# Kernel optimization log

Measured on AMD Instinct MI355X. Metric: run time of the kernel, lower is better.

Reference implementation:

```python
import jax, jax.numpy as jnp
import numpy as np

TEMPERATURE = 0.1
NORM_EPS = 1e-12          # F.normalize default eps
SMALL_VAL = float(np.finfo(np.float32).tiny)  # pytorch-metric-learning small_val(float32)
NEG_INF = float(np.finfo(np.float32).min)     # c_f.neg_inf for masked logsumexp


def setup_inputs() -> dict:
    key = jax.random.key(0)
    k1, k2 = jax.random.split(key)
    N, D = 8192, 128
    emb = jax.random.normal(k1, (N, D), dtype=jnp.float32)
    labels = jax.random.randint(k2, (N,), 0, 1000, dtype=jnp.int64)
    return {"emb": emb, "labels": labels}


def reference(emb, labels):
    N = emb.shape[0]
    # F.normalize(emb, dim=1): x / max(||x||, eps)
    norms = jnp.linalg.norm(emb, axis=1, keepdims=True)
    x = emb / jnp.maximum(norms, NORM_EPS)

    # cosine similarity matrix [N, N], scaled by temperature
    mat = jnp.matmul(x, x.T) / TEMPERATURE

    same = labels[:, None] == labels[None, :]
    diag = jnp.eye(N, dtype=bool)
    pos_mask = same & ~diag          # same label, i != j
    keep_mask = ~diag                # pos + neg (all off-diagonal)

    # numerical stability: subtract detached row max (over full row, incl. diagonal)
    mat_max = jax.lax.stop_gradient(jnp.max(mat, axis=1, keepdims=True))
    mat = mat - mat_max

    # masked logsumexp over off-diagonal entries
    masked = jnp.where(keep_mask, mat, NEG_INF)
    denom = jax.nn.logsumexp(masked, axis=1, keepdims=True)  # [N, 1]

    log_prob = mat - denom
    pos_f = pos_mask.astype(mat.dtype)
    mean_log_prob_pos = jnp.sum(pos_f * log_prob, axis=1) / (
        jnp.sum(pos_f, axis=1) + SMALL_VAL
    )
    losses = -mean_log_prob_pos  # per-element losses
    # SumReducer: sum over elements
    return jnp.sum(losses)
```

## Files before the change

kernel.cpp:

```cpp
#include <hip/hip_runtime.h>
#include <hip/hip_bf16.h>


typedef __bf16 bf16_t;
typedef __bf16 bf16x2 __attribute__((ext_vector_type(2)));
typedef __bf16 bf16x8 __attribute__((ext_vector_type(8)));
typedef float f32x16 __attribute__((ext_vector_type(16)));

#define NN 8192
#define DIM 128
#define NB 256
#define SEGS 32
#define SMALL_VAL 1.17549435e-38f
#define L2E10 14.4269504089f
#define LN2 0.69314718056f

__device__ inline size_t swz(int row, int lane) {
    int f = lane >> 3, hh = (lane >> 2) & 1, j = (lane & 3) << 1;
    return ((size_t)(row >> 5) * 4096) + f * 512 + hh * 256 + (row & 31) * 8 + j;
}

__global__ __launch_bounds__(256) void norm_csum(const float* __restrict__ emb,
                                                 const int* __restrict__ labels,
                                                 bf16_t* __restrict__ xsw,
                                                 float* __restrict__ cd_arr,
                                                 float* __restrict__ sd_arr,
                                                 float* __restrict__ cm1_arr,
                                                 float* __restrict__ se_acc,
                                                 float* __restrict__ out) {
    __shared__ float cs[DIM];
    __shared__ int rowlist[96];
    __shared__ int nrows;
    int cls = blockIdx.x;
    int wv = threadIdx.x >> 6, lane = threadIdx.x & 63;
    if (threadIdx.x < DIM) cs[threadIdx.x] = 0.f;
    if (threadIdx.x == 0) nrows = 0;
    if (threadIdx.x < 8) se_acc[cls * 8 + threadIdx.x] = 0.f;
    if (cls == 0 && threadIdx.x == 0) *out = 0.f;
    __syncthreads();

    float s0 = 0.f, s1 = 0.f;
    const int4* lab4 = (const int4*)(labels + wv * 2048);
#pragma unroll
    for (int it = 0; it < 8; ++it) {
        int4 l = lab4[it * 64 + lane];
        int base = wv * 2048 + it * 256;
#pragma unroll
        for (int cmp = 0; cmp < 4; ++cmp) {
            int li = (cmp == 0) ? l.x : (cmp == 1) ? l.y : (cmp == 2) ? l.z : l.w;
            unsigned long long m = __ballot(li == cls);
            while (m) {
                int bb = __builtin_ctzll(m);
                m &= m - 1;
                int row = base + 4 * bb + cmp;
                float2 v = ((const float2*)emb)[row * 64 + lane];
                float ss = fmaf(v.x, v.x, v.y * v.y);
#pragma unroll
                for (int mm = 1; mm < 64; mm <<= 1) ss += __shfl_xor(ss, mm, 64);
                float inv = 1.0f / fmaxf(sqrtf(ss), 1e-12f);
                bf16x2 o; o.x = (bf16_t)(v.x * inv); o.y = (bf16_t)(v.y * inv);
                *(bf16x2*)(xsw + swz(row, lane)) = o;
                s0 += (float)o.x; s1 += (float)o.y;
                if (lane == 0) {
                    int idx = atomicAdd(&nrows, 1);
                    if (idx < 96) rowlist[idx] = row;
                }
            }
        }
    }
    atomicAdd(&cs[2 * lane], s0);
    atomicAdd(&cs[2 * lane + 1], s1);
    __syncthreads();
    int n = nrows;
    for (int k = wv; k < n; k += 4) {
        int row = rowlist[k];
        bf16x2 xv = *(const bf16x2*)(xsw + swz(row, lane));
        float x0 = (float)xv.x, x1 = (float)xv.y;
        float cdp = fmaf(x0, cs[2 * lane], x1 * cs[2 * lane + 1]);
        float sdp = fmaf(x0, x0, x1 * x1);
#pragma unroll
        for (int mm = 1; mm < 64; mm <<= 1) {
            cdp += __shfl_xor(cdp, mm, 64);
            sdp += __shfl_xor(sdp, mm, 64);
        }
        if (lane == 0) {
            cd_arr[row] = cdp; sd_arr[row] = sdp; cm1_arr[row] = (float)(n - 1);
        }
    }
}

__global__ __launch_bounds__(256, 4) void main_kernel(const bf16_t* __restrict__ xsw,
                                                      float* __restrict__ se_acc) {
    int wid  = blockIdx.x * 4 + (threadIdx.x >> 6);
    int lane = threadIdx.x & 63;
    int I = wid >> 5, s = wid & 31;
    int NT = NB - I;
    int t0 = (NT * s) >> 5, t1 = (NT * (s + 1)) >> 5;
    if (t0 == t1) return;

    int c = lane & 31, h = lane >> 5;
    int laneoff = h * 256 + c * 8;

    const bf16_t* abase = xsw + (size_t)I * 4096 + laneoff;
    bf16x8 a[8];
#pragma unroll
    for (int f = 0; f < 8; ++f) a[f] = *(const bf16x8*)(abase + f * 512);

    float se[16];
#pragma unroll
    for (int r = 0; r < 16; ++r) se[r] = 0.f;

    for (int t = t0; t < t1; ++t) {
        int J = I + t;
        const bf16_t* bbase = xsw + (size_t)J * 4096 + laneoff;
        bf16x8 b[8];
#pragma unroll
        for (int f = 0; f < 8; ++f) b[f] = *(const bf16x8*)(bbase + f * 512);
        f32x16 acc;
#pragma unroll
        for (int r = 0; r < 16; ++r) acc[r] = 0.f;
#pragma unroll
        for (int f = 0; f < 8; ++f)
            acc = __builtin_amdgcn_mfma_f32_32x32x16_bf16(a[f], b[f], acc, 0, 0, 0);

        if (J == I) {
#pragma unroll
            for (int r = 0; r < 16; ++r) {
                bool isdiag = c == ((r & 3) + 8 * (r >> 2) + 4 * h);
                float e = isdiag ? 0.f
                                 : __builtin_amdgcn_exp2f(fmaf(acc[r], L2E10, -L2E10));
                se[r] += e;
            }
        } else {
            float c0 = 0.f, c1 = 0.f, c2 = 0.f, c3 = 0.f;
#pragma unroll
            for (int r = 0; r < 16; ++r) {
                float e = __builtin_amdgcn_exp2f(fmaf(acc[r], L2E10, -L2E10));
                se[r] += e;
                if ((r & 3) == 0) c0 += e; else if ((r & 3) == 1) c1 += e;
                else if ((r & 3) == 2) c2 += e; else c3 += e;
            }
            float v = (c0 + c1) + (c2 + c3);
            v += __shfl_xor(v, 32, 64);
            if (h == 0) atomicAdd(&se_acc[J * 32 + c], v);
        }
    }

#pragma unroll
    for (int r = 0; r < 16; ++r) {
        float vv = se[r];
#pragma unroll
        for (int m = 1; m < 32; m <<= 1) vv += __shfl_xor(vv, m, 64);
        se[r] = vv;
    }
    if (c == 0) {
        int rowbase = I * 32 + 4 * h;
#pragma unroll
        for (int r = 0; r < 16; ++r)
            atomicAdd(&se_acc[rowbase + (r & 3) + 8 * (r >> 2)], se[r]);
    }
}

__global__ __launch_bounds__(256) void finalize_kernel(const float* __restrict__ se_acc,
                                                       const float* __restrict__ cd_arr,
                                                       const float* __restrict__ sd_arr,
                                                       const float* __restrict__ cm1_arr,
                                                       float* __restrict__ out) {
    __shared__ float part[4];
    int i = blockIdx.x * 256 + threadIdx.x;
    float sd = sd_arr[i], cd = cd_arr[i], cm1 = cm1_arr[i];
    float sev  = fmaxf(se_acc[i], 1e-30f);
    float lse  = fmaf(__builtin_amdgcn_logf(sev), LN2, 10.f);
    float loss = (cm1 * lse - 10.f * (cd - sd)) / (cm1 + SMALL_VAL);
#pragma unroll
    for (int m = 1; m < 64; m <<= 1) loss += __shfl_xor(loss, m, 64);
    int wv = threadIdx.x >> 6;
    if ((threadIdx.x & 63) == 0) part[wv] = loss;
    __syncthreads();
    if (threadIdx.x == 0) atomicAdd(out, part[0] + part[1] + part[2] + part[3]);
}

extern "C" void kernel_launch(void* const* d_in, const int* in_sizes, int n_in,
                              void* d_out, int out_size, void* d_ws, size_t ws_size,
                              hipStream_t stream) {
    const float* emb  = (const float*)d_in[0];
    const int* labels = (const int*)d_in[1];

    char* ws = (char*)d_ws;
    bf16_t* xsw = (bf16_t*)ws;
    float* se   = (float*)(ws + (size_t)NN * DIM * 2);
    float* cd   = se + NN;
    float* sd   = cd + NN;
    float* cm1  = sd + NN;

    norm_csum<<<1024, 256, 0, stream>>>(emb, labels, xsw, cd, sd, cm1, se, (float*)d_out);
    main_kernel<<<NB * SEGS / 4, 256, 0, stream>>>(xsw, se);
    finalize_kernel<<<NN / 256, 256, 0, stream>>>(se, cd, sd, cm1, (float*)d_out);
}
```

Baseline: 103.2 us.

## Fuse finalize into main kernel via last-block reduction and double-buffer B loads

The separate finalize kernel is removed. Each main_kernel block increments a done counter, and the last block to finish computes the per-row loss and writes the sum, which saves one kernel launch. The loop over B tiles now uses two register buffers so the next tile's global loads are in flight while the current MFMA and exp work runs. Launch bounds drop from 4 to 3 blocks per CU to make room for the extra registers, at the cost of occupancy, and the final reduction now runs serially on a single block.

```diff
diff --git a/kernel.cpp b/kernel.cpp
--- a/kernel.cpp
+++ b/kernel.cpp
@@ -11,6 +11,7 @@
 #define DIM 128
 #define NB 256
 #define SEGS 32
+#define NBLK (NB * SEGS / 4)
 #define SMALL_VAL 1.17549435e-38f
 #define L2E10 14.4269504089f
 #define LN2 0.69314718056f
@@ -27,7 +28,7 @@
                                                  float* __restrict__ sd_arr,
                                                  float* __restrict__ cm1_arr,
                                                  float* __restrict__ se_acc,
-                                                 float* __restrict__ out) {
+                                                 int* __restrict__ done) {
     __shared__ float cs[DIM];
     __shared__ int rowlist[96];
     __shared__ int nrows;
@@ -36,7 +37,7 @@
     if (threadIdx.x < DIM) cs[threadIdx.x] = 0.f;
     if (threadIdx.x == 0) nrows = 0;
     if (threadIdx.x < 8) se_acc[cls * 8 + threadIdx.x] = 0.f;
-    if (cls == 0 && threadIdx.x == 0) *out = 0.f;
+    if (cls == 0 && threadIdx.x == 0) *done = 0;
     __syncthreads();
 
     float s0 = 0.f, s1 = 0.f;
@@ -89,95 +90,114 @@
     }
 }
 
-__global__ __launch_bounds__(256, 4) void main_kernel(const bf16_t* __restrict__ xsw,
-                                                      float* __restrict__ se_acc) {
+#define LDB(dst, J_) do {                                                        \
+    const bf16_t* p_ = xsw + (size_t)(J_) * 4096 + laneoff;                      \
+    _Pragma("unroll")                                                            \
+    for (int f_ = 0; f_ < 8; ++f_) dst[f_] = *(const bf16x8*)(p_ + f_ * 512);    \
+} while (0)
+
+#define TILE(bb, J_) do {                                                        \
+    f32x16 acc_;                                                                 \
+    _Pragma("unroll")                                                            \
+    for (int r_ = 0; r_ < 16; ++r_) acc_[r_] = 0.f;                              \
+    _Pragma("unroll")                                                            \
+    for (int f_ = 0; f_ < 8; ++f_)                                               \
+        acc_ = __builtin_amdgcn_mfma_f32_32x32x16_bf16(a[f_], bb[f_], acc_, 0, 0, 0); \
+    if ((J_) == I) {                        \
+        _Pragma("unroll")                                                        \
+        for (int r_ = 0; r_ < 16; ++r_) {                                        \
+            bool isd_ = c == ((r_ & 3) + 8 * (r_ >> 2) + 4 * h);                 \
+            se[r_] += isd_ ? 0.f                                                 \
+                           : __builtin_amdgcn_exp2f(fmaf(acc_[r_], L2E10, -L2E10)); \
+        }                                                                        \
+    } else {                                \
+        float c0_=0.f, c1_=0.f, c2_=0.f, c3_=0.f;                                \
+        _Pragma("unroll")                                                        \
+        for (int r_ = 0; r_ < 16; ++r_) {                                        \
+            float e_ = __builtin_amdgcn_exp2f(fmaf(acc_[r_], L2E10, -L2E10));    \
+            se[r_] += e_;                                                        \
+            if ((r_&3)==0) c0_+=e_; else if ((r_&3)==1) c1_+=e_;                 \
+            else if ((r_&3)==2) c2_+=e_; else c3_+=e_;                           \
+        }                                                                        \
+        float v_ = (c0_ + c1_) + (c2_ + c3_);                                    \
+        v_ += __shfl_xor(v_, 32, 64);                                            \
+        if (h == 0) atomicAdd(&se_acc[(J_) * 32 + c], v_);                       \
+    }                                                                            \
+} while (0)
+
+__global__ __launch_bounds__(256, 3) void main_kernel(const bf16_t* __restrict__ xsw,
+                                                      const float* __restrict__ cd_arr,
+                                                      const float* __restrict__ sd_arr,
+                                                      const float* __restrict__ cm1_arr,
+                                                      float* __restrict__ se_acc,
+                                                      int* __restrict__ done,
+                                                      float* __restrict__ out) {
+    __shared__ float part[4];
+    __shared__ int amlast;
     int wid  = blockIdx.x * 4 + (threadIdx.x >> 6);
     int lane = threadIdx.x & 63;
     int I = wid >> 5, s = wid & 31;
     int NT = NB - I;
     int t0 = (NT * s) >> 5, t1 = (NT * (s + 1)) >> 5;
-    if (t0 == t1) return;
-
     int c = lane & 31, h = lane >> 5;
     int laneoff = h * 256 + c * 8;
 
-    const bf16_t* abase = xsw + (size_t)I * 4096 + laneoff;
-    bf16x8 a[8];
-#pragma unroll
-    for (int f = 0; f < 8; ++f) a[f] = *(const bf16x8*)(abase + f * 512);
-
-    float se[16];
-#pragma unroll
-    for (int r = 0; r < 16; ++r) se[r] = 0.f;
-
-    for (int t = t0; t < t1; ++t) {
-        int J = I + t;
-        const bf16_t* bbase = xsw + (size_t)J * 4096 + laneoff;
-        bf16x8 b[8];
-#pragma unroll
-        for (int f = 0; f < 8; ++f) b[f] = *(const bf16x8*)(bbase + f * 512);
-        f32x16 acc;
-#pragma unroll
-        for (int r = 0; r < 16; ++r) acc[r] = 0.f;
-#pragma unroll
-        for (int f = 0; f < 8; ++f)
-            acc = __builtin_amdgcn_mfma_f32_32x32x16_bf16(a[f], b[f], acc, 0, 0, 0);
-
-        if (J == I) {
-#pragma unroll
-            for (int r = 0; r < 16; ++r) {
-                bool isdiag = c == ((r & 3) + 8 * (r >> 2) + 4 * h);
-                float e = isdiag ? 0.f
-                                 : __builtin_amdgcn_exp2f(fmaf(acc[r], L2E10, -L2E10));
-                se[r] += e;
-            }
-        } else {
-            float c0 = 0.f, c1 = 0.f, c2 = 0.f, c3 = 0.f;
-#pragma unroll
-            for (int r = 0; r < 16; ++r) {
-                float e = __builtin_amdgcn_exp2f(fmaf(acc[r], L2E10, -L2E10));
-                se[r] += e;
-                if ((r & 3) == 0) c0 += e; else if ((r & 3) == 1) c1 += e;
-                else if ((r & 3) == 2) c2 += e; else c3 += e;
-            }
-            float v = (c0 + c1) + (c2 + c3);
-            v += __shfl_xor(v, 32, 64);
-            if (h == 0) atomicAdd(&se_acc[J * 32 + c], v);
-        }
-    }
-
-#pragma unroll
-    for (int r = 0; r < 16; ++r) {
-        float vv = se[r];
-#pragma unroll
-        for (int m = 1; m < 32; m <<= 1) vv += __shfl_xor(vv, m, 64);
-        se[r] = vv;
-    }
-    if (c == 0) {
-        int rowbase = I * 32 + 4 * h;
-#pragma unroll
-        for (int r = 0; r < 16; ++r)
-            atomicAdd(&se_acc[rowbase + (r & 3) + 8 * (r >> 2)], se[r]);
-    }
-}
-
-__global__ __launch_bounds__(256) void finalize_kernel(const float* __restrict__ se_acc,
-                                                       const float* __restrict__ cd_arr,
-                                                       const float* __restrict__ sd_arr,
-                                                       const float* __restrict__ cm1_arr,
-                                                       float* __restrict__ out) {
-    __shared__ float part[4];
-    int i = blockIdx.x * 256 + threadIdx.x;
-    float sd = sd_arr[i], cd = cd_arr[i], cm1 = cm1_arr[i];
-    float sev  = fmaxf(se_acc[i], 1e-30f);
-    float lse  = fmaf(__builtin_amdgcn_logf(sev), LN2, 10.f);
-    float loss = (cm1 * lse - 10.f * (cd - sd)) / (cm1 + SMALL_VAL);
-#pragma unroll
-    for (int m = 1; m < 64; m <<= 1) loss += __shfl_xor(loss, m, 64);
-    int wv = threadIdx.x >> 6;
-    if ((threadIdx.x & 63) == 0) part[wv] = loss;
-    __syncthreads();
-    if (threadIdx.x == 0) atomicAdd(out, part[0] + part[1] + part[2] + part[3]);
+    if (t0 < t1) {
+        const bf16_t* abase = xsw + (size_t)I * 4096 + laneoff;
+        bf16x8 a[8];
+#pragma unroll
+        for (int f = 0; f < 8; ++f) a[f] = *(const bf16x8*)(abase + f * 512);
+
+        float se[16];
+#pragma unroll
+        for (int r = 0; r < 16; ++r) se[r] = 0.f;
+
+        bf16x8 b0[8], b1[8];
+        int t = t0;
+        LDB(b0, I + t);
+        while (t + 1 < t1) {
+            LDB(b1, I + t + 1);
+            TILE(b0, I + t);
+            if (t + 2 < t1) LDB(b0, I + t + 2);
+            TILE(b1, I + t + 1);
+            t += 2;
+        }
+        if (t < t1) TILE(b0, I + t);
+
+#pragma unroll
+        for (int r = 0; r < 16; ++r) {
+            float vv = se[r];
+#pragma unroll
+            for (int m = 1; m < 32; m <<= 1) vv += __shfl_xor(vv, m, 64);
+            se[r] = vv;
+        }
+        if (c == 0) {
+            int rowbase = I * 32 + 4 * h;
+#pragma unroll
+            for (int r = 0; r < 16; ++r)
+                atomicAdd(&se_acc[rowbase + (r & 3) + 8 * (r >> 2)], se[r]);
+        }
+    }
+
+    __syncthreads();
+    if (threadIdx.x == 0) amlast = (atomicAdd(done, 1) == NBLK - 1);
+    __syncthreads();
+    if (!amlast) return;
+
+    float lsum = 0.f;
+    for (int i = threadIdx.x; i < NN; i += 256) {
+        float sev = __hip_atomic_load(&se_acc[i], __ATOMIC_RELAXED,
+                                      __HIP_MEMORY_SCOPE_AGENT);
+        float sd = sd_arr[i], cd = cd_arr[i], cm1 = cm1_arr[i];
+        sev = fmaxf(sev, 1e-30f);
+        float lse = fmaf(__builtin_amdgcn_logf(sev), LN2, 10.f);
+        lsum += (cm1 * lse - 10.f * (cd - sd)) / (cm1 + SMALL_VAL);
+    }
+#pragma unroll
+    for (int m = 1; m < 64; m <<= 1) lsum += __shfl_xor(lsum, m, 64);
+    if (lane == 0) part[threadIdx.x >> 6] = lsum;
+    __syncthreads();
+    if (threadIdx.x == 0) *out = part[0] + part[1] + part[2] + part[3];
 }
 
 extern "C" void kernel_launch(void* const* d_in, const int* in_sizes, int n_in,
@@ -192,8 +212,8 @@
     float* cd   = se + NN;
     float* sd   = cd + NN;
     float* cm1  = sd + NN;
-
-    norm_csum<<<1024, 256, 0, stream>>>(emb, labels, xsw, cd, sd, cm1, se, (float*)d_out);
-    main_kernel<<<NB * SEGS / 4, 256, 0, stream>>>(xsw, se);
-    finalize_kernel<<<NN / 256, 256, 0, stream>>>(se, cd, sd, cm1, (float*)d_out);
-}
+    int*   done = (int*)(cm1 + NN);
+
+    norm_csum<<<1024, 256, 0, stream>>>(emb, labels, xsw, cd, sd, cm1, se, done);
+    main_kernel<<<NBLK, 256, 0, stream>>>(xsw, cd, sd, cm1, se, done, (float*)d_out);
+}
```

After: 117.1 us. 13.5% more time.

## Compute full similarity matrix per row block instead of exploiting symmetry

Applied to the files above, without the earlier changes.

The main kernel stops using the upper-triangular symmetric schedule, where each off-diagonal tile also fed column sums through global atomics. Now each wave owns one 32-row block and sweeps 16 fixed column tiles, and the grid covers the full 256x256 tile space with row-only accumulation. This removes the per-tile column atomics, the shuffles and the uneven triangular split across waves. In exchange, roughly twice as many MFMA tiles and exp evaluations run, and the loop is unrolled by two.

```diff
diff --git a/kernel.cpp b/kernel.cpp
--- a/kernel.cpp
+++ b/kernel.cpp
@@ -10,7 +10,7 @@
 #define NN 8192
 #define DIM 128
 #define NB 256
-#define SEGS 32
+#define SEGS 16
 #define SMALL_VAL 1.17549435e-38f
 #define L2E10 14.4269504089f
 #define LN2 0.69314718056f
@@ -91,13 +91,9 @@
 
 __global__ __launch_bounds__(256, 4) void main_kernel(const bf16_t* __restrict__ xsw,
                                                       float* __restrict__ se_acc) {
-    int wid  = blockIdx.x * 4 + (threadIdx.x >> 6);
-    int lane = threadIdx.x & 63;
-    int I = wid >> 5, s = wid & 31;
-    int NT = NB - I;
-    int t0 = (NT * s) >> 5, t1 = (NT * (s + 1)) >> 5;
-    if (t0 == t1) return;
-
+    int wv = threadIdx.x >> 6, lane = threadIdx.x & 63;
+    int s = blockIdx.x >> 6;
+    int I = (blockIdx.x & 63) * 4 + wv;
     int c = lane & 31, h = lane >> 5;
     int laneoff = h * 256 + c * 8;
 
@@ -110,9 +106,10 @@
 #pragma unroll
     for (int r = 0; r < 16; ++r) se[r] = 0.f;
 
-    for (int t = t0; t < t1; ++t) {
-        int J = I + t;
-        const bf16_t* bbase = xsw + (size_t)J * 4096 + laneoff;
+    int j0 = s * 16;
+#pragma unroll 2
+    for (int jt = j0; jt < j0 + 16; ++jt) {
+        const bf16_t* bbase = xsw + (size_t)jt * 4096 + laneoff;
         bf16x8 b[8];
 #pragma unroll
         for (int f = 0; f < 8; ++f) b[f] = *(const bf16x8*)(bbase + f * 512);
@@ -123,26 +120,17 @@
         for (int f = 0; f < 8; ++f)
             acc = __builtin_amdgcn_mfma_f32_32x32x16_bf16(a[f], b[f], acc, 0, 0, 0);
 
-        if (J == I) {
+        if (jt == I) {
 #pragma unroll
             for (int r = 0; r < 16; ++r) {
                 bool isdiag = c == ((r & 3) + 8 * (r >> 2) + 4 * h);
-                float e = isdiag ? 0.f
-                                 : __builtin_amdgcn_exp2f(fmaf(acc[r], L2E10, -L2E10));
-                se[r] += e;
+                se[r] += isdiag ? 0.f
+                                : __builtin_amdgcn_exp2f(fmaf(acc[r], L2E10, -L2E10));
             }
         } else {
-            float c0 = 0.f, c1 = 0.f, c2 = 0.f, c3 = 0.f;
 #pragma unroll
-            for (int r = 0; r < 16; ++r) {
-                float e = __builtin_amdgcn_exp2f(fmaf(acc[r], L2E10, -L2E10));
-                se[r] += e;
-                if ((r & 3) == 0) c0 += e; else if ((r & 3) == 1) c1 += e;
-                else if ((r & 3) == 2) c2 += e; else c3 += e;
-            }
-            float v = (c0 + c1) + (c2 + c3);
-            v += __shfl_xor(v, 32, 64);
-            if (h == 0) atomicAdd(&se_acc[J * 32 + c], v);
+            for (int r = 0; r < 16; ++r)
+                se[r] += __builtin_amdgcn_exp2f(fmaf(acc[r], L2E10, -L2E10));
         }
     }
 
@@ -194,6 +182,6 @@
     float* cm1  = sd + NN;
 
     norm_csum<<<1024, 256, 0, stream>>>(emb, labels, xsw, cd, sd, cm1, se, (float*)d_out);
-    main_kernel<<<NB * SEGS / 4, 256, 0, stream>>>(xsw, se);
+    main_kernel<<<NB / 4 * SEGS, 256, 0, stream>>>(xsw, se);
     finalize_kernel<<<NN / 256, 256, 0, stream>>>(se, cd, sd, cm1, (float*)d_out);
 }
```

Measured after the change: 99.42 us. 3.7% less time.
